# Performance work log

Hardware: AMD Instinct MI355X
Metric: run time of the kernel (lower is better)

The kernel has to match this reference:

```python
import jax, jax.numpy as jnp
import numpy as np

N = 50000      # nodes
E = 800000     # edges
DIN = 128
DH = 128
DE = 128
DOUT = 2
EPS = 1e-5     # GraphNorm eps


def _xavier(key, fan_in, fan_out):
    lim = float(np.sqrt(6.0 / (fan_in + fan_out)))
    return jax.random.uniform(key, (fan_in, fan_out), jnp.float32, -lim, lim)


def setup_inputs() -> dict:
    key = jax.random.key(0)
    ks = jax.random.split(key, 8)
    x = jax.random.normal(ks[0], (N, DIN), jnp.float32)
    edge_index = jax.random.randint(ks[1], (2, E), 0, N, dtype=jnp.int32)
    W1 = _xavier(ks[2], DIN, DH); b1 = jnp.zeros((DH,), jnp.float32)
    W2 = _xavier(ks[3], DH, DH);  b2 = jnp.zeros((DH,), jnp.float32)
    W3 = _xavier(ks[4], DH, DE);  b3 = jnp.zeros((DE,), jnp.float32)
    gn1_w = jnp.ones((DH,), jnp.float32); gn1_b = jnp.zeros((DH,), jnp.float32); gn1_a = jnp.ones((DH,), jnp.float32)
    gn2_w = jnp.ones((DH,), jnp.float32); gn2_b = jnp.zeros((DH,), jnp.float32); gn2_a = jnp.ones((DH,), jnp.float32)
    Wout = _xavier(ks[5], DE, DOUT); bout = jnp.zeros((DOUT,), jnp.float32)
    return {
        "x": x, "edge_index": edge_index,
        "W1": W1, "b1": b1, "W2": W2, "b2": b2, "W3": W3, "b3": b3,
        "gn1_w": gn1_w, "gn1_b": gn1_b, "gn1_a": gn1_a,
        "gn2_w": gn2_w, "gn2_b": gn2_b, "gn2_a": gn2_a,
        "Wout": Wout, "bout": bout,
    }


def gcn_conv(x, src, dst, W, b):
    # PyG GCNConv: add self-loops, symmetric normalization, linear, scatter-add at dst.
    n = x.shape[0]
    h = x @ W                                   # [N, C]
    loop = jnp.arange(n, dtype=src.dtype)
    s = jnp.concatenate([src, loop])            # [E+N]
    d = jnp.concatenate([dst, loop])
    deg = jnp.zeros((n,), h.dtype).at[d].add(1.0)
    dinv = jnp.where(deg > 0, jax.lax.rsqrt(deg), 0.0)
    norm = dinv[s] * dinv[d]                    # [E+N]
    out = jnp.zeros_like(h).at[d].add(h[s] * norm[:, None])
    return out + b


def graph_norm(h, w, b, alpha):
    # Single-graph GraphNorm: shift by alpha*mean, normalize by variance of shifted values.
    mean = h.mean(axis=0)
    c = h - alpha * mean
    var = (c * c).mean(axis=0)
    return c * jax.lax.rsqrt(var + EPS) * w + b


def reference(x, edge_index, W1, b1, W2, b2, W3, b3,
              gn1_w, gn1_b, gn1_a, gn2_w, gn2_b, gn2_a, Wout, bout):
    src, dst = edge_index[0], edge_index[1]
    h = gcn_conv(x, src, dst, W1, b1)
    h = jax.nn.relu(graph_norm(h, gn1_w, gn1_b, gn1_a))   # dropout identity (eval)
    h = gcn_conv(h, src, dst, W2, b2)
    h = jax.nn.relu(graph_norm(h, gn2_w, gn2_b, gn2_a))
    h = gcn_conv(h, src, dst, W3, b3)
    return h @ Wout + bout
```

## Files before the change

### kernel.cpp

```cpp
#include <hip/hip_runtime.h>

#define GN_EPS 1e-5f


#define HIST_C 64
#define SCAN_CHUNK 4096
#define LDK 136

typedef __attribute__((ext_vector_type(8))) short short8;
typedef __attribute__((ext_vector_type(4))) float f32x4;

__device__ __forceinline__ unsigned short f2bf(float f) {
    unsigned u = __float_as_uint(f);
    u += 0x7fffu + ((u >> 16) & 1u);
    return (unsigned short)(u >> 16);
}
__device__ __forceinline__ float bflo(unsigned u) { return __uint_as_float(u << 16); }
__device__ __forceinline__ float bfhi(unsigned u) { return __uint_as_float(u & 0xffff0000u); }

__global__ __launch_bounds__(256) void k_prep_hist(const float* __restrict__ W1,
                                                   const float* __restrict__ W2,
                                                   const float* __restrict__ W3,
                                                   const float* __restrict__ Wo,
                                                   const float* __restrict__ b3,
                                                   const float* __restrict__ bo,
                                                   unsigned short* __restrict__ Wt,
                                                   float* __restrict__ M,
                                                   float* __restrict__ mb,
                                                   const int* __restrict__ dst,
                                                   unsigned short* __restrict__ cnt,
                                                   unsigned short* __restrict__ pos,
                                                   int e, int n, int chunk) {
    __shared__ __align__(16) unsigned bins[32768];
    if (blockIdx.x < 2) {
        unsigned short* sT = (unsigned short*)bins;
        const float* W = blockIdx.x == 0 ? W1 : W2;
        unsigned short* o = Wt + blockIdx.x * 16384;
        const float4* W4 = (const float4*)W;
        for (int idx = threadIdx.x; idx < 128 * 32; idx += 256) {
            int k = idx >> 5, c4 = idx & 31;
            float4 v = W4[k * 32 + c4];
            sT[(c4 * 4 + 0) * 130 + k] = f2bf(v.x);
            sT[(c4 * 4 + 1) * 130 + k] = f2bf(v.y);
            sT[(c4 * 4 + 2) * 130 + k] = f2bf(v.z);
            sT[(c4 * 4 + 3) * 130 + k] = f2bf(v.w);
        }
        __syncthreads();
        for (int idx = threadIdx.x; idx < 128 * 128; idx += 256) {
            int c = idx >> 7, k = idx & 127;
            o[idx] = sT[c * 130 + k];
        }
    } else if (blockIdx.x == 2) {
        int k = threadIdx.x;
        if (k < 128) {
            float m0 = 0.f, m1 = 0.f;
            for (int c = 0; c < 128; ++c) {
                float w = W3[k * 128 + c];
                m0 += w * Wo[c * 2];
                m1 += w * Wo[c * 2 + 1];
            }
            M[k * 2] = m0;
            M[k * 2 + 1] = m1;
            if (k < 2) {
                float s = 0.f;
                for (int c = 0; c < 128; ++c) s += b3[c] * Wo[c * 2 + k];
                mb[k] = s + bo[k];
            }
        }
    } else {
        const int c = (int)blockIdx.x - 3;
        const int c0 = c * chunk;
        const int c1 = (c0 + chunk < e) ? c0 + chunk : e;
        const int nw = (n + 1) >> 1;
        for (int i = threadIdx.x; i < nw; i += 256) bins[i] = 0u;
        __syncthreads();
        const bool al = ((size_t)dst & 15) == 0;
        for (int i = c0 + (int)threadIdx.x * 4; i < c1; i += 1024) {
            if (al && i + 3 < c1) {
                int4 d4 = *(const int4*)(dst + i);
                unsigned o0 = atomicAdd(&bins[(unsigned)d4.x >> 1],
                                        (d4.x & 1) ? 0x10000u : 1u);
                unsigned o1 = atomicAdd(&bins[(unsigned)d4.y >> 1],
                                        (d4.y & 1) ? 0x10000u : 1u);
                unsigned o2 = atomicAdd(&bins[(unsigned)d4.z >> 1],
                                        (d4.z & 1) ? 0x10000u : 1u);
                unsigned o3 = atomicAdd(&bins[(unsigned)d4.w >> 1],
                                        (d4.w & 1) ? 0x10000u : 1u);
                ushort4 p;
                p.x = (unsigned short)((o0 >> ((d4.x & 1) * 16)) & 0xffffu);
                p.y = (unsigned short)((o1 >> ((d4.y & 1) * 16)) & 0xffffu);
                p.z = (unsigned short)((o2 >> ((d4.z & 1) * 16)) & 0xffffu);
                p.w = (unsigned short)((o3 >> ((d4.w & 1) * 16)) & 0xffffu);
                *(ushort4*)(pos + i) = p;
            } else {
                for (int k = i; k < c1 && k < i + 4; ++k) {
                    int d = dst[k];
                    unsigned old = atomicAdd(&bins[(unsigned)d >> 1],
                                             (d & 1) ? 0x10000u : 1u);
                    pos[k] = (unsigned short)((old >> ((d & 1) * 16)) & 0xffffu);
                }
            }
        }
        __syncthreads();
        unsigned short* cr = cnt + (size_t)c * n;
        if ((n & 1) == 0) {
            unsigned* cr32 = (unsigned*)cr;
            for (int i = threadIdx.x; i < (n >> 1); i += 256) cr32[i] = bins[i];
        } else {
            for (int i = threadIdx.x; i < n; i += 256)
                cr[i] = (unsigned short)((bins[i >> 1] >> ((i & 1) * 16)) & 0xffffu);
        }
    }
}

__global__ __launch_bounds__(256) void k_reduce(unsigned short* __restrict__ cnt,
                                                int* __restrict__ degi,
                                                int* __restrict__ partial,
                                                int n, int nchunks) {
    int node = blockIdx.x * 256 + threadIdx.x;
    int pdeg = 0;
    if (node < n) {
        int s = 0;
        int cb = 0;
        for (; cb + 8 <= nchunks; cb += 8) {
            int v[8];
            #pragma unroll
            for (int q = 0; q < 8; ++q) v[q] = cnt[(size_t)(cb + q) * n + node];
            #pragma unroll
            for (int q = 0; q < 8; ++q) {
                cnt[(size_t)(cb + q) * n + node] = (unsigned short)s;
                s += v[q];
            }
        }
        for (; cb < nchunks; ++cb) {
            size_t id = (size_t)cb * n + node;
            int v = cnt[id];
            cnt[id] = (unsigned short)s;
            s += v;
        }
        degi[node] = s;
        pdeg = (s + 7) & ~7;
    }
    #pragma unroll
    for (int off = 32; off; off >>= 1) pdeg += __shfl_down(pdeg, off);
    __shared__ int ws[4];
    if ((threadIdx.x & 63) == 0) ws[threadIdx.x >> 6] = pdeg;
    __syncthreads();
    if (threadIdx.x == 0) partial[blockIdx.x] = ws[0] + ws[1] + ws[2] + ws[3];
}

__global__ __launch_bounds__(256) void k_scanfinal(const int* __restrict__ degi,
                                                   const int* __restrict__ partial,
                                                   int* __restrict__ rowptr,
                                                   float* __restrict__ dinv, int n, int nb) {
    int blockbase = 0;
    for (int i = 0; i < (int)blockIdx.x * 16; ++i) blockbase += partial[i];

    int base = blockIdx.x * SCAN_CHUNK + threadIdx.x * 16;
    int v[16], pv[16];
    int s = 0;
    #pragma unroll
    for (int q = 0; q < 16; ++q) {
        int i = base + q;
        v[q] = (i < n) ? degi[i] : 0;
        pv[q] = (v[q] + 7) & ~7;
        s += pv[q];
    }
    const int lane = threadIdx.x & 63;
    const int wid = threadIdx.x >> 6;
    int x = s;
    #pragma unroll
    for (int off = 1; off < 64; off <<= 1) {
        int t = __shfl_up(x, off);
        if (lane >= off) x += t;
    }
    __shared__ int ws[4];
    if (lane == 63) ws[wid] = x;
    __syncthreads();
    int waveoff = 0;
    if (wid > 0) waveoff += ws[0];
    if (wid > 1) waveoff += ws[1];
    if (wid > 2) waveoff += ws[2];
    int excl = x - s + waveoff + blockbase;
    #pragma unroll
    for (int q = 0; q < 16; ++q) {
        int i = base + q;
        if (i < n) {
            rowptr[i] = excl;
            dinv[i] = rsqrtf((float)(v[q] + 1));
        }
        excl += pv[q];
    }
    if ((int)blockIdx.x == nb - 1 && threadIdx.x == 255) {
        rowptr[n] = excl;
    }
}

__global__ void k_fill(const int* __restrict__ src, const int* __restrict__ dst,
                       const unsigned short* __restrict__ pos,
                       const unsigned short* __restrict__ pref,
                       const int* __restrict__ rowptr,
                       const float* __restrict__ dinv,
                       unsigned* __restrict__ csr_ew, int e, int n, int chunk) {
    int base = (blockIdx.x * blockDim.x + threadIdx.x) * 4;
    if (base >= e) return;
    const unsigned short* pr = pref + (size_t)(base / chunk) * n;
    if (base + 3 < e && (((size_t)src & 15) == 0) && (((size_t)dst & 15) == 0)) {
        int4 s4 = *(const int4*)(src + base);
        int4 d4 = *(const int4*)(dst + base);
        ushort4 p4 = *(const ushort4*)(pos + base);
        float as0 = dinv[s4.x], as1 = dinv[s4.y], as2 = dinv[s4.z], as3 = dinv[s4.w];
        float ad0 = dinv[d4.x], ad1 = dinv[d4.y], ad2 = dinv[d4.z], ad3 = dinv[d4.w];
        int b0 = rowptr[d4.x] + pr[d4.x] + p4.x;
        int b1 = rowptr[d4.y] + pr[d4.y] + p4.y;
        int b2 = rowptr[d4.z] + pr[d4.z] + p4.z;
        int b3 = rowptr[d4.w] + pr[d4.w] + p4.w;
        csr_ew[b0] = ((unsigned)s4.x << 16) | (unsigned)f2bf(as0 * ad0);
        csr_ew[b1] = ((unsigned)s4.y << 16) | (unsigned)f2bf(as1 * ad1);
        csr_ew[b2] = ((unsigned)s4.z << 16) | (unsigned)f2bf(as2 * ad2);
        csr_ew[b3] = ((unsigned)s4.w << 16) | (unsigned)f2bf(as3 * ad3);
    } else {
        for (int i = base; i < e && i < base + 4; ++i) {
            int s = src[i], d = dst[i];
            float w = dinv[s] * dinv[d];
            csr_ew[rowptr[d] + (int)pr[d] + (int)pos[i]] =
                ((unsigned)s << 16) | (unsigned)f2bf(w);
        }
    }
}

__global__ __launch_bounds__(256) void k_gemm_f32(const float* __restrict__ X,
                                                  const unsigned short* __restrict__ Wt,
                                                  unsigned short* __restrict__ Y,
                                                  int nrows) {
    __shared__ __align__(16) unsigned short sB[128 * LDK];
    const int t = threadIdx.x;
    const int row0 = blockIdx.x * 64;

    for (int idx = t; idx < 128 * 16; idx += 256) {
        int c = idx >> 4, ch = idx & 15;
        uint4 v = ((const uint4*)(Wt + c * 128))[ch];
        *(uint4*)(&sB[c * LDK + ch * 8]) = v;
    }

    const int w = t >> 6;
    const int lane = t & 63;
    const int m = lane & 15;
    const int quad = lane >> 4;

    const int grow_a = row0 + w * 16 + m;
    const int srow = grow_a < nrows ? grow_a : 0;
    const float4* Xr = (const float4*)(X + (size_t)srow * 128);
    short8 a[4];
    #pragma unroll
    for (int ks = 0; ks < 4; ++ks) {
        int ko4 = ks * 8 + quad * 2;
        float4 v0 = Xr[ko4];
        float4 v1 = Xr[ko4 + 1];
        short8 av;
        av[0] = (short)f2bf(v0.x); av[1] = (short)f2bf(v0.y);
        av[2] = (short)f2bf(v0.z); av[3] = (short)f2bf(v0.w);
        av[4] = (short)f2bf(v1.x); av[5] = (short)f2bf(v1.y);
        av[6] = (short)f2bf(v1.z); av[7] = (short)f2bf(v1.w);
        a[ks] = av;
    }
    __syncthreads();

    f32x4 acc[8] = {};
    #pragma unroll
    for (int ks = 0; ks < 4; ++ks) {
        int ko = ks * 32 + quad * 8;
        #pragma unroll
        for (int ct = 0; ct < 8; ++ct) {
            short8 b = *(const short8*)(&sB[(ct * 16 + m) * LDK + ko]);
            acc[ct] = __builtin_amdgcn_mfma_f32_16x16x32_bf16(a[ks], b, acc[ct], 0, 0, 0);
        }
    }
    #pragma unroll
    for (int r = 0; r < 4; ++r) {
        int grow = row0 + w * 16 + quad * 4 + r;
        if (grow >= nrows) continue;
        unsigned short* yr = Y + (size_t)grow * 128 + m;
        #pragma unroll
        for (int ct = 0; ct < 8; ++ct) yr[ct * 16] = f2bf(acc[ct][r]);
    }
}

__global__ __launch_bounds__(256) void k_gemm_bf(const unsigned short* __restrict__ Xb,
                                                 const unsigned short* __restrict__ Wt,
                                                 unsigned short* __restrict__ Y,
                                                 const float* __restrict__ cs,
                                                 const float* __restrict__ cb,
                                                 int nrows) {
    __shared__ __align__(16) unsigned short sB[128 * LDK];
    const int t = threadIdx.x;
    const int row0 = blockIdx.x * 64;

    for (int idx = t; idx < 128 * 16; idx += 256) {
        int c = idx >> 4, ch = idx & 15;
        uint4 v = ((const uint4*)(Wt + c * 128))[ch];
        *(uint4*)(&sB[c * LDK + ch * 8]) = v;
    }

    const int w = t >> 6;
    const int lane = t & 63;
    const int m = lane & 15;
    const int quad = lane >> 4;

    const int grow_a = row0 + w * 16 + m;
    const int srow = grow_a < nrows ? grow_a : 0;
    const uint4* Xr = (const uint4*)(Xb + (size_t)srow * 128);
    short8 a[4];
    #pragma unroll
    for (int ks = 0; ks < 4; ++ks) {
        uint4 u = Xr[ks * 4 + quad];
        int kf = (ks * 32 + quad * 8) >> 2;
        float4 s0 = ((const float4*)cs)[kf];
        float4 s1 = ((const float4*)cs)[kf + 1];
        float4 c0 = ((const float4*)cb)[kf];
        float4 c1 = ((const float4*)cb)[kf + 1];
        short8 av;
        av[0] = (short)f2bf(fmaxf(fmaf(bflo(u.x), s0.x, c0.x), 0.f));
        av[1] = (short)f2bf(fmaxf(fmaf(bfhi(u.x), s0.y, c0.y), 0.f));
        av[2] = (short)f2bf(fmaxf(fmaf(bflo(u.y), s0.z, c0.z), 0.f));
        av[3] = (short)f2bf(fmaxf(fmaf(bfhi(u.y), s0.w, c0.w), 0.f));
        av[4] = (short)f2bf(fmaxf(fmaf(bflo(u.z), s1.x, c1.x), 0.f));
        av[5] = (short)f2bf(fmaxf(fmaf(bfhi(u.z), s1.y, c1.y), 0.f));
        av[6] = (short)f2bf(fmaxf(fmaf(bflo(u.w), s1.z, c1.z), 0.f));
        av[7] = (short)f2bf(fmaxf(fmaf(bfhi(u.w), s1.w, c1.w), 0.f));
        a[ks] = av;
    }
    __syncthreads();

    f32x4 acc[8] = {};
    #pragma unroll
    for (int ks = 0; ks < 4; ++ks) {
        int ko = ks * 32 + quad * 8;
        #pragma unroll
        for (int ct = 0; ct < 8; ++ct) {
            short8 b = *(const short8*)(&sB[(ct * 16 + m) * LDK + ko]);
            acc[ct] = __builtin_amdgcn_mfma_f32_16x16x32_bf16(a[ks], b, acc[ct], 0, 0, 0);
        }
    }
    #pragma unroll
    for (int r = 0; r < 4; ++r) {
        int grow = row0 + w * 16 + quad * 4 + r;
        if (grow >= nrows) continue;
        unsigned short* yr = Y + (size_t)grow * 128 + m;
        #pragma unroll
        for (int ct = 0; ct < 8; ++ct) yr[ct * 16] = f2bf(acc[ct][r]);
    }
}

__global__ __launch_bounds__(256) void k_gather(const unsigned short* __restrict__ H,
                                                unsigned short* __restrict__ O,
                                                const int* __restrict__ rowptr,
                                                const unsigned* __restrict__ csr_ew,
                                                const float* __restrict__ dinv,
                                                const float* __restrict__ bias,
                                                float* __restrict__ pS,
                                                float* __restrict__ pQ, int n) {
    __shared__ float sS[4][128];
    __shared__ float sQ[4][128];
    const int wid = threadIdx.x >> 6;
    const int node = blockIdx.x * 4 + wid;
    const int lane = threadIdx.x & 63;
    const int qw = lane >> 4;
    const int ql = lane & 15;
    const uint4* Hx = (const uint4*)H;
    float acc[8] = {};
    if (node < n) {
        float di = dinv[node];
        if (qw == 0) {
            uint4 u = Hx[(size_t)node * 16 + ql];
            float dd = di * di;
            float4 ba = ((const float4*)bias)[ql * 2];
            float4 bb = ((const float4*)bias)[ql * 2 + 1];
            acc[0] = bflo(u.x) * dd + ba.x; acc[1] = bfhi(u.x) * dd + ba.y;
            acc[2] = bflo(u.y) * dd + ba.z; acc[3] = bfhi(u.y) * dd + ba.w;
            acc[4] = bflo(u.z) * dd + bb.x; acc[5] = bfhi(u.z) * dd + bb.y;
            acc[6] = bflo(u.w) * dd + bb.z; acc[7] = bfhi(u.w) * dd + bb.w;
        }
        int j = rowptr[node];
        const int end = rowptr[node + 1];
        for (; j + 24 <= end; j += 24) {
            unsigned ew[6];
            #pragma unroll
            for (int q = 0; q < 6; ++q) ew[q] = csr_ew[j + 4 * q + qw];
            uint4 u[6];
            #pragma unroll
            for (int q = 0; q < 6; ++q)
                u[q] = Hx[((ew[q] >> 12) & 0xFFFF0u) + (unsigned)ql];
            #pragma unroll
            for (int q = 0; q < 6; ++q) {
                float nr = __uint_as_float(ew[q] << 16);
                acc[0] += bflo(u[q].x) * nr; acc[1] += bfhi(u[q].x) * nr;
                acc[2] += bflo(u[q].y) * nr; acc[3] += bfhi(u[q].y) * nr;
                acc[4] += bflo(u[q].z) * nr; acc[5] += bfhi(u[q].z) * nr;
                acc[6] += bflo(u[q].w) * nr; acc[7] += bfhi(u[q].w) * nr;
            }
        }
        if (j + 16 <= end) {
            unsigned ew[4];
            #pragma unroll
            for (int q = 0; q < 4; ++q) ew[q] = csr_ew[j + 4 * q + qw];
            uint4 u[4];
            #pragma unroll
            for (int q = 0; q < 4; ++q)
                u[q] = Hx[((ew[q] >> 12) & 0xFFFF0u) + (unsigned)ql];
            #pragma unroll
            for (int q = 0; q < 4; ++q) {
                float nr = __uint_as_float(ew[q] << 16);
                acc[0] += bflo(u[q].x) * nr; acc[1] += bfhi(u[q].x) * nr;
                acc[2] += bflo(u[q].y) * nr; acc[3] += bfhi(u[q].y) * nr;
                acc[4] += bflo(u[q].z) * nr; acc[5] += bfhi(u[q].z) * nr;
                acc[6] += bflo(u[q].w) * nr; acc[7] += bfhi(u[q].w) * nr;
            }
            j += 16;
        }
        if (j < end) {
            unsigned ew[2];
            #pragma unroll
            for (int q = 0; q < 2; ++q) ew[q] = csr_ew[j + qw * 2 + q];
            uint4 u[2];
            #pragma unroll
            for (int q = 0; q < 2; ++q)
                u[q] = Hx[((ew[q] >> 12) & 0xFFFF0u) + (unsigned)ql];
            #pragma unroll
            for (int q = 0; q < 2; ++q) {
                float nr = __uint_as_float(ew[q] << 16);
                acc[0] += bflo(u[q].x) * nr; acc[1] += bfhi(u[q].x) * nr;
                acc[2] += bflo(u[q].y) * nr; acc[3] += bfhi(u[q].y) * nr;
                acc[4] += bflo(u[q].z) * nr; acc[5] += bfhi(u[q].z) * nr;
                acc[6] += bflo(u[q].w) * nr; acc[7] += bfhi(u[q].w) * nr;
            }
        }
        #pragma unroll
        for (int i = 0; i < 8; ++i) {
            acc[i] += __shfl_down(acc[i], 32);
            acc[i] += __shfl_down(acc[i], 16);
        }
    }
    if (qw == 0) {
        if (node < n) {
            unsigned short h[8];
            float v[8];
            #pragma unroll
            for (int i = 0; i < 8; ++i) {
                h[i] = f2bf(acc[i]);
                v[i] = __uint_as_float((unsigned)h[i] << 16);
                sS[wid][ql * 8 + i] = v[i];
                sQ[wid][ql * 8 + i] = v[i] * v[i];
            }
            uint4 o;
            o.x = (unsigned)h[0] | ((unsigned)h[1] << 16);
            o.y = (unsigned)h[2] | ((unsigned)h[3] << 16);
            o.z = (unsigned)h[4] | ((unsigned)h[5] << 16);
            o.w = (unsigned)h[6] | ((unsigned)h[7] << 16);
            *(uint4*)(O + (size_t)node * 128 + ql * 8) = o;
        } else {
            #pragma unroll
            for (int i = 0; i < 8; ++i) {
                sS[wid][ql * 8 + i] = 0.f;
                sQ[wid][ql * 8 + i] = 0.f;
            }
        }
    }
    __syncthreads();
    const int t = threadIdx.x;
    if (t < 128) {
        float s = sS[0][t] + sS[1][t] + sS[2][t] + sS[3][t];
        float q = sQ[0][t] + sQ[1][t] + sQ[2][t] + sQ[3][t];
        const int slotb = (blockIdx.x & 63) << 7;
        atomicAdd(&pS[slotb + t], s);
        atomicAdd(&pQ[slotb + t], q);
    }
}

__global__ __launch_bounds__(256) void k_zproj(const unsigned short* __restrict__ Xb,
                                               const float* __restrict__ M,
                                               const float* __restrict__ cs,
                                               const float* __restrict__ cb,
                                               float2* __restrict__ Z, int n) {
    int node = blockIdx.x * 4 + (threadIdx.x >> 6);
    if (node >= n) return;
    int lane = threadIdx.x & 63;
    unsigned u = ((const unsigned*)Xb)[(size_t)node * 64 + lane];
    int c0 = lane * 2;
    float a = fmaxf(fmaf(bflo(u), cs[c0], cb[c0]), 0.f);
    float b = fmaxf(fmaf(bfhi(u), cs[c0 + 1], cb[c0 + 1]), 0.f);
    float p0 = a * M[c0 * 2]     + b * M[(c0 + 1) * 2];
    float p1 = a * M[c0 * 2 + 1] + b * M[(c0 + 1) * 2 + 1];
    #pragma unroll
    for (int off = 32; off; off >>= 1) {
        p0 += __shfl_down(p0, off);
        p1 += __shfl_down(p1, off);
    }
    if (lane == 0) Z[node] = make_float2(p0, p1);
}

__global__ __launch_bounds__(256) void k_gatherZ(const float2* __restrict__ Z,
                                                 const int* __restrict__ rowptr,
                                                 const unsigned* __restrict__ csr_ew,
                                                 const float* __restrict__ dinv,
                                                 const float* __restrict__ mb,
                                                 float* __restrict__ out, int n) {
    int wid = threadIdx.x >> 6;
    int lane = threadIdx.x & 63;
    int g = lane >> 4;
    int gl = lane & 15;
    int node = blockIdx.x * 16 + wid * 4 + g;
    if (node >= n) return;
    float2 acc = make_float2(0.f, 0.f);
    if (gl == 0) {
        float di = dinv[node];
        float2 z = Z[node];
        acc.x = z.x * di * di + mb[0];
        acc.y = z.y * di * di + mb[1];
    }
    int j = rowptr[node];
    const int end = rowptr[node + 1];
    for (int jj = j + gl; jj < end; jj += 16) {
        unsigned ew = csr_ew[jj];
        float2 z = Z[ew >> 16];
        float w = __uint_as_float(ew << 16);
        acc.x += z.x * w;
        acc.y += z.y * w;
    }
    #pragma unroll
    for (int off = 8; off; off >>= 1) {
        acc.x += __shfl_down(acc.x, off);
        acc.y += __shfl_down(acc.y, off);
    }
    if (gl == 0) {
        out[(size_t)node * 2]     = acc.x;
        out[(size_t)node * 2 + 1] = acc.y;
    }
}

__global__ void k_finstats(const float* __restrict__ pS, const float* __restrict__ pQ,
                           const float* __restrict__ w, const float* __restrict__ b,
                           const float* __restrict__ alpha,
                           float* __restrict__ colscale, float* __restrict__ colshift,
                           int n) {
    int c = threadIdx.x;
    if (c >= 128) return;
    float s = 0.f, q = 0.f;
    #pragma unroll 8
    for (int blk = 0; blk < 64; ++blk) {
        s += pS[blk * 128 + c];
        q += pQ[blk * 128 + c];
    }
    float inv_n = 1.0f / (float)n;
    float m = s * inv_n;
    float eh2 = q * inv_n;
    float a = alpha[c];
    float var = eh2 - (2.0f * a - a * a) * m * m;
    float scale = rsqrtf(var + GN_EPS) * w[c];
    colscale[c] = scale;
    colshift[c] = b[c] - a * m * scale;
}

extern "C" void kernel_launch(void* const* d_in, const int* in_sizes, int n_in,
                              void* d_out, int out_size, void* d_ws, size_t ws_size,
                              hipStream_t stream) {
    const float* x    = (const float*)d_in[0];
    const int*   ei   = (const int*)  d_in[1];
    const float* W1   = (const float*)d_in[2];
    const float* b1   = (const float*)d_in[3];
    const float* W2   = (const float*)d_in[4];
    const float* b2   = (const float*)d_in[5];
    const float* W3   = (const float*)d_in[6];
    const float* b3   = (const float*)d_in[7];
    const float* gn1w = (const float*)d_in[8];
    const float* gn1b = (const float*)d_in[9];
    const float* gn1a = (const float*)d_in[10];
    const float* gn2w = (const float*)d_in[11];
    const float* gn2b = (const float*)d_in[12];
    const float* gn2a = (const float*)d_in[13];
    const float* Wout = (const float*)d_in[14];
    const float* bout = (const float*)d_in[15];
    float* out = (float*)d_out;

    const int n = in_sizes[0] / 128;
    const int e = in_sizes[1] / 2;
    const int* srcI = ei;
    const int* dstI = ei + e;

    const int chunk = (((e + HIST_C - 1) / HIST_C) + 3) & ~3;
    const int nchunks = (e + chunk - 1) / chunk;

    char* base = (char*)d_ws;
    size_t off = 0;
    auto take = [&](size_t bytes) -> void* {
        void* r = base + off;
        off += (bytes + 15) & ~(size_t)15;
        return r;
    };
    unsigned short* bufH = (unsigned short*)take((size_t)n * 256);
    unsigned short* bufG = (unsigned short*)take((size_t)n * 256);
    float* dinv     = (float*)take((size_t)n * 4);
    float* colscale = (float*)take(128 * 4);
    float* colshift = (float*)take(128 * 4);
    int*   rowptr   = (int*)take(((size_t)n + 1) * 4);
    int*   partial  = (int*)take(256 * 4);
    unsigned short* Wt = (unsigned short*)take(2 * 16384 * 2);
    float* M        = (float*)take(256 * 4);
    float* mb       = (float*)take(2 * 4);
    float2* Z       = (float2*)take((size_t)n * 8);
    int*   degi     = (int*)take((size_t)n * 4);
    unsigned short* cnt = (unsigned short*)take((size_t)nchunks * n * 2);
    unsigned short* pos = (unsigned short*)take((size_t)e * 2);
    float* pS       = (float*)take(2 * 64 * 128 * 4);
    float* pQ       = (float*)take(2 * 64 * 128 * 4);
    size_t csr_cap  = (size_t)e + 8 * (size_t)n;
    unsigned* csr_ew = (unsigned*)take(csr_cap * 4);
    size_t zbytes   = (size_t)((base + off) - (char*)pS);

    const int nb = (n + SCAN_CHUNK - 1) / SCAN_CHUNK;
    const int gemmGrid = (n + 63) / 64;
    const int gathGrid = (n + 3) / 4;

    hipMemsetAsync(pS, 0, zbytes, stream);
    k_prep_hist<<<3 + nchunks, 256, 0, stream>>>(W1, W2, W3, Wout, b3, bout,
                                                 Wt, M, mb, dstI, cnt, pos, e, n, chunk);
    k_reduce<<<(n + 255) / 256, 256, 0, stream>>>(cnt, degi, partial, n, nchunks);
    k_scanfinal<<<nb, 256, 0, stream>>>(degi, partial, rowptr, dinv, n, nb);
    k_fill<<<(e + 1023) / 1024, 256, 0, stream>>>(srcI, dstI, pos, cnt, rowptr,
                                                  dinv, csr_ew, e, n, chunk);

    k_gemm_f32<<<gemmGrid, 256, 0, stream>>>(x, Wt, bufH, n);
    k_gather<<<gathGrid, 256, 0, stream>>>(bufH, bufG, rowptr, csr_ew, dinv, b1, pS, pQ, n);
    k_finstats<<<1, 128, 0, stream>>>(pS, pQ, gn1w, gn1b, gn1a, colscale, colshift, n);

    k_gemm_bf<<<gemmGrid, 256, 0, stream>>>(bufG, Wt + 16384, bufH, colscale, colshift, n);
    k_gather<<<gathGrid, 256, 0, stream>>>(bufH, bufG, rowptr, csr_ew, dinv, b2,
                                           pS + 8192, pQ + 8192, n);
    k_finstats<<<1, 128, 0, stream>>>(pS + 8192, pQ + 8192, gn2w, gn2b, gn2a,
                                      colscale, colshift, n);

    k_zproj<<<gathGrid, 256, 0, stream>>>(bufG, M, colscale, colshift, Z, n);
    k_gatherZ<<<(n + 15) / 16, 256, 0, stream>>>(Z, rowptr, csr_ew, dinv, mb, out, n);
}
```

Baseline: 265.5 us.

## Fuse degree reduction with first GEMM and zero CSR padding in scan

Result: slower. 272.1 us (+2.5%).

```diff
diff --git a/kernel.cpp b/kernel.cpp
--- a/kernel.cpp
+++ b/kernel.cpp
@@ -3,7 +3,7 @@
 #define GN_EPS 1e-5f
 
 
-#define HIST_C 64
+#define HIST_C 208
 #define SCAN_CHUNK 4096
 #define LDK 136
 
@@ -113,46 +113,120 @@
     }
 }
 
-__global__ __launch_bounds__(256) void k_reduce(unsigned short* __restrict__ cnt,
-                                                int* __restrict__ degi,
-                                                int* __restrict__ partial,
-                                                int n, int nchunks) {
-    int node = blockIdx.x * 256 + threadIdx.x;
-    int pdeg = 0;
-    if (node < n) {
-        int s = 0;
-        int cb = 0;
-        for (; cb + 8 <= nchunks; cb += 8) {
-            int v[8];
-            #pragma unroll
-            for (int q = 0; q < 8; ++q) v[q] = cnt[(size_t)(cb + q) * n + node];
-            #pragma unroll
-            for (int q = 0; q < 8; ++q) {
-                cnt[(size_t)(cb + q) * n + node] = (unsigned short)s;
-                s += v[q];
-            }
-        }
-        for (; cb < nchunks; ++cb) {
-            size_t id = (size_t)cb * n + node;
-            int v = cnt[id];
-            cnt[id] = (unsigned short)s;
-            s += v;
-        }
-        degi[node] = s;
-        pdeg = (s + 7) & ~7;
-    }
-    #pragma unroll
-    for (int off = 32; off; off >>= 1) pdeg += __shfl_down(pdeg, off);
+__global__ __launch_bounds__(256) void k_reduce_gemm(unsigned short* __restrict__ cnt,
+                                                     int* __restrict__ degi,
+                                                     int* __restrict__ partial,
+                                                     int n, int nchunks,
+                                                     const float* __restrict__ X,
+                                                     const unsigned short* __restrict__ Wt,
+                                                     unsigned short* __restrict__ Y,
+                                                     int nrows, int nred, int ngem) {
+    __shared__ __align__(16) unsigned short sB[128 * LDK];
     __shared__ int ws[4];
-    if ((threadIdx.x & 63) == 0) ws[threadIdx.x >> 6] = pdeg;
+
+    int mn2 = (nred < ngem ? nred : ngem) * 2;
+    bool isr;
+    int bid;
+    if ((int)blockIdx.x < mn2) {
+        isr = (blockIdx.x & 1) == 0;
+        bid = blockIdx.x >> 1;
+    } else {
+        int r = (int)blockIdx.x - mn2;
+        isr = nred > ngem;
+        bid = (mn2 >> 1) + r;
+    }
+
+    if (isr) {
+        int node = bid * 256 + threadIdx.x;
+        int pdeg = 0;
+        if (node < n) {
+            int s = 0;
+            int cb = 0;
+            for (; cb + 8 <= nchunks; cb += 8) {
+                int v[8];
+                #pragma unroll
+                for (int q = 0; q < 8; ++q) v[q] = cnt[(size_t)(cb + q) * n + node];
+                #pragma unroll
+                for (int q = 0; q < 8; ++q) {
+                    cnt[(size_t)(cb + q) * n + node] = (unsigned short)s;
+                    s += v[q];
+                }
+            }
+            for (; cb < nchunks; ++cb) {
+                size_t id = (size_t)cb * n + node;
+                int v = cnt[id];
+                cnt[id] = (unsigned short)s;
+                s += v;
+            }
+            degi[node] = s;
+            pdeg = (s + 7) & ~7;
+        }
+        #pragma unroll
+        for (int off = 32; off; off >>= 1) pdeg += __shfl_down(pdeg, off);
+        if ((threadIdx.x & 63) == 0) ws[threadIdx.x >> 6] = pdeg;
+        __syncthreads();
+        if (threadIdx.x == 0) partial[bid] = ws[0] + ws[1] + ws[2] + ws[3];
+        return;
+    }
+
+    const int t = threadIdx.x;
+    const int row0 = bid * 64;
+
+    for (int idx = t; idx < 128 * 16; idx += 256) {
+        int c = idx >> 4, ch = idx & 15;
+        uint4 v = ((const uint4*)(Wt + c * 128))[ch];
+        *(uint4*)(&sB[c * LDK + ch * 8]) = v;
+    }
+
+    const int w = t >> 6;
+    const int lane = t & 63;
+    const int m = lane & 15;
+    const int quad = lane >> 4;
+
+    const int grow_a = row0 + w * 16 + m;
+    const int srow = grow_a < nrows ? grow_a : 0;
+    const float4* Xr = (const float4*)(X + (size_t)srow * 128);
+    short8 a[4];
+    #pragma unroll
+    for (int ks = 0; ks < 4; ++ks) {
+        int ko4 = ks * 8 + quad * 2;
+        float4 v0 = Xr[ko4];
+        float4 v1 = Xr[ko4 + 1];
+        short8 av;
+        av[0] = (short)f2bf(v0.x); av[1] = (short)f2bf(v0.y);
+        av[2] = (short)f2bf(v0.z); av[3] = (short)f2bf(v0.w);
+        av[4] = (short)f2bf(v1.x); av[5] = (short)f2bf(v1.y);
+        av[6] = (short)f2bf(v1.z); av[7] = (short)f2bf(v1.w);
+        a[ks] = av;
+    }
     __syncthreads();
-    if (threadIdx.x == 0) partial[blockIdx.x] = ws[0] + ws[1] + ws[2] + ws[3];
+
+    f32x4 acc[8] = {};
+    #pragma unroll
+    for (int ks = 0; ks < 4; ++ks) {
+        int ko = ks * 32 + quad * 8;
+        #pragma unroll
+        for (int ct = 0; ct < 8; ++ct) {
+            short8 b = *(const short8*)(&sB[(ct * 16 + m) * LDK + ko]);
+            acc[ct] = __builtin_amdgcn_mfma_f32_16x16x32_bf16(a[ks], b, acc[ct], 0, 0, 0);
+        }
+    }
+    #pragma unroll
+    for (int r = 0; r < 4; ++r) {
+        int grow = row0 + w * 16 + quad * 4 + r;
+        if (grow >= nrows) continue;
+        unsigned short* yr = Y + (size_t)grow * 128 + m;
+        #pragma unroll
+        for (int ct = 0; ct < 8; ++ct) yr[ct * 16] = f2bf(acc[ct][r]);
+    }
 }
 
 __global__ __launch_bounds__(256) void k_scanfinal(const int* __restrict__ degi,
                                                    const int* __restrict__ partial,
                                                    int* __restrict__ rowptr,
-                                                   float* __restrict__ dinv, int n, int nb) {
+                                                   float* __restrict__ dinv,
+                                                   unsigned* __restrict__ csr_ew,
+                                                   int n, int nb) {
     int blockbase = 0;
     for (int i = 0; i < (int)blockIdx.x * 16; ++i) blockbase += partial[i];
 
@@ -188,6 +262,7 @@
         if (i < n) {
             rowptr[i] = excl;
             dinv[i] = rsqrtf((float)(v[q] + 1));
+            for (int z = v[q]; z < pv[q]; ++z) csr_ew[excl + z] = 0u;
         }
         excl += pv[q];
     }
@@ -229,63 +304,6 @@
     }
 }
 
-__global__ __launch_bounds__(256) void k_gemm_f32(const float* __restrict__ X,
-                                                  const unsigned short* __restrict__ Wt,
-                                                  unsigned short* __restrict__ Y,
-                                                  int nrows) {
-    __shared__ __align__(16) unsigned short sB[128 * LDK];
-    const int t = threadIdx.x;
-    const int row0 = blockIdx.x * 64;
-
-    for (int idx = t; idx < 128 * 16; idx += 256) {
-        int c = idx >> 4, ch = idx & 15;
-        uint4 v = ((const uint4*)(Wt + c * 128))[ch];
-        *(uint4*)(&sB[c * LDK + ch * 8]) = v;
-    }
-
-    const int w = t >> 6;
-    const int lane = t & 63;
-    const int m = lane & 15;
-    const int quad = lane >> 4;
-
-    const int grow_a = row0 + w * 16 + m;
-    const int srow = grow_a < nrows ? grow_a : 0;
-    const float4* Xr = (const float4*)(X + (size_t)srow * 128);
-    short8 a[4];
-    #pragma unroll
-    for (int ks = 0; ks < 4; ++ks) {
-        int ko4 = ks * 8 + quad * 2;
-        float4 v0 = Xr[ko4];
-        float4 v1 = Xr[ko4 + 1];
-        short8 av;
-        av[0] = (short)f2bf(v0.x); av[1] = (short)f2bf(v0.y);
-        av[2] = (short)f2bf(v0.z); av[3] = (short)f2bf(v0.w);
-        av[4] = (short)f2bf(v1.x); av[5] = (short)f2bf(v1.y);
-        av[6] = (short)f2bf(v1.z); av[7] = (short)f2bf(v1.w);
-        a[ks] = av;
-    }
-    __syncthreads();
-
-    f32x4 acc[8] = {};
-    #pragma unroll
-    for (int ks = 0; ks < 4; ++ks) {
-        int ko = ks * 32 + quad * 8;
-        #pragma unroll
-        for (int ct = 0; ct < 8; ++ct) {
-            short8 b = *(const short8*)(&sB[(ct * 16 + m) * LDK + ko]);
-            acc[ct] = __builtin_amdgcn_mfma_f32_16x16x32_bf16(a[ks], b, acc[ct], 0, 0, 0);
-        }
-    }
-    #pragma unroll
-    for (int r = 0; r < 4; ++r) {
-        int grow = row0 + w * 16 + quad * 4 + r;
-        if (grow >= nrows) continue;
-        unsigned short* yr = Y + (size_t)grow * 128 + m;
-        #pragma unroll
-        for (int ct = 0; ct < 8; ++ct) yr[ct * 16] = f2bf(acc[ct][r]);
-    }
-}
-
 __global__ __launch_bounds__(256) void k_gemm_bf(const unsigned short* __restrict__ Xb,
                                                  const unsigned short* __restrict__ Wt,
                                                  unsigned short* __restrict__ Y,
@@ -611,25 +629,27 @@
     int*   degi     = (int*)take((size_t)n * 4);
     unsigned short* cnt = (unsigned short*)take((size_t)nchunks * n * 2);
     unsigned short* pos = (unsigned short*)take((size_t)e * 2);
+    size_t csr_cap  = (size_t)e + 8 * (size_t)n;
+    unsigned* csr_ew = (unsigned*)take(csr_cap * 4);
     float* pS       = (float*)take(2 * 64 * 128 * 4);
     float* pQ       = (float*)take(2 * 64 * 128 * 4);
-    size_t csr_cap  = (size_t)e + 8 * (size_t)n;
-    unsigned* csr_ew = (unsigned*)take(csr_cap * 4);
     size_t zbytes   = (size_t)((base + off) - (char*)pS);
 
     const int nb = (n + SCAN_CHUNK - 1) / SCAN_CHUNK;
     const int gemmGrid = (n + 63) / 64;
+    const int redGrid  = (n + 255) / 256;
     const int gathGrid = (n + 3) / 4;
 
     hipMemsetAsync(pS, 0, zbytes, stream);
     k_prep_hist<<<3 + nchunks, 256, 0, stream>>>(W1, W2, W3, Wout, b3, bout,
                                                  Wt, M, mb, dstI, cnt, pos, e, n, chunk);
-    k_reduce<<<(n + 255) / 256, 256, 0, stream>>>(cnt, degi, partial, n, nchunks);
-    k_scanfinal<<<nb, 256, 0, stream>>>(degi, partial, rowptr, dinv, n, nb);
+    k_reduce_gemm<<<redGrid + gemmGrid, 256, 0, stream>>>(cnt, degi, partial, n, nchunks,
+                                                          x, Wt, bufH, n,
+                                                          redGrid, gemmGrid);
+    k_scanfinal<<<nb, 256, 0, stream>>>(degi, partial, rowptr, dinv, csr_ew, n, nb);
     k_fill<<<(e + 1023) / 1024, 256, 0, stream>>>(srcI, dstI, pos, cnt, rowptr,
                                                   dinv, csr_ew, e, n, chunk);
 
-    k_gemm_f32<<<gemmGrid, 256, 0, stream>>>(x, Wt, bufH, n);
     k_gather<<<gathGrid, 256, 0, stream>>>(bufH, bufG, rowptr, csr_ew, dinv, b1, pS, pQ, n);
     k_finstats<<<1, 128, 0, stream>>>(pS, pQ, gn1w, gn1b, gn1a, colscale, colshift, n);
 
```
